# Optimization experiments

Measured on AMD Instinct MI355X. Metric: run time of the kernel, lower is better.

The kernel has to match this reference:

```python
import jax, jax.numpy as jnp
import numpy as np

BUFFER_SIZE = 1024
N_BANDS = 2049
N_SPEC = 4
FRAME_SIZE = 2 * (N_BANDS - 1)  # 4096
EPS = 1e-10


def _hann_periodic(n):
    k = np.arange(n, dtype=np.float64)
    return (0.5 * (1.0 - np.cos(2.0 * np.pi * k / n))).astype(np.float32)


def _build_windows():
    # Mirrors _build_windows with nonlinearity=0 (single filterbank).
    base = _hann_periodic(FRAME_SIZE) / (FRAME_SIZE / 4.0)
    win_scale = float(base.sum())
    wins = [base.copy()]
    for lvl in range(1, N_SPEC):
        stride = 1 << lvl
        small = base[::stride][: FRAME_SIZE // stride]
        w = np.zeros(FRAME_SIZE, dtype=np.float32)
        w[-(FRAME_SIZE // stride):] = small
        w *= win_scale / w.sum()
        wins.append(w)
    return [jnp.asarray(w) for w in wins]


WINDOWS = _build_windows()


def _forward(x):
    # x: (B, BUFFER_SIZE). Fresh (reset) state: time buffers are zeros,
    # spectrogram/left-boundary buffers are +1e6 (identity for min).
    B = x.shape[0]
    T = 1 << (N_SPEC - 1)  # finest time grid = output columns
    out = jnp.full((B, N_BANDS, T), 1.0e6, dtype=x.dtype)
    pad = jnp.zeros((B, FRAME_SIZE), dtype=x.dtype)
    concat = jnp.concatenate([pad, x], axis=-1)  # (B, FRAME_SIZE + BUFFER_SIZE)
    for lvl in range(N_SPEC):
        chunk = BUFFER_SIZE >> lvl
        nfr = 1 << lvl  # sub-frames at this level
        # Overlap-save sliding windows: frame i starts at offset chunk + i*chunk
        frames = jnp.stack(
            [concat[:, chunk + i * chunk: chunk + i * chunk + FRAME_SIZE] for i in range(nfr)],
            axis=1,
        )  # (B, nfr, FRAME_SIZE)
        spec = jnp.fft.rfft(frames * WINDOWS[lvl][None, None, :], n=FRAME_SIZE, axis=-1)
        power = jnp.transpose(spec.real ** 2 + spec.imag ** 2, (0, 2, 1))  # (B, N_BANDS, nfr)
        # Upsample coarse-time levels to the finest grid (tile replication, the
        # streaming moving-max/min buffers realize this in the original) and
        # take the min across scales (buffers initialised to 1e6 = +inf for min).
        out = jnp.minimum(out, jnp.repeat(power, T // nfr, axis=-1))
    return 10.0 * jnp.log10(jnp.maximum(out, EPS))  # power -> dB


def setup_inputs() -> dict:
    key = jax.random.key(0)
    x = jax.random.normal(key, (1024, BUFFER_SIZE), dtype=jnp.float32)
    return {"x": x}


def reference(x):
    return _forward(x)
```

## Files before the change

### kernel.cpp

```cpp
#include <hip/hip_runtime.h>
#include <hip/hip_fp16.h>
#include <math.h>

#define NBANDS 2049
#define NF 4096
#define NC 2048
#define BUF 1024
#define THREADS 512
#define R2C 0.70710678118654752f

__device__ __forceinline__ int SW(int i) { return i ^ (i >> 2) ^ (i >> 6); }

__device__ __forceinline__ int posrev10(int j) {
  return ((j & 3) << 9) | (((j >> 2) & 3) << 7) | (((j >> 4) & 3) << 5) |
         (((j >> 6) & 3) << 3) | (((j >> 8) & 3) << 1);
}

struct Smem {
  alignas(16) float xs[BUF];
  alignas(16) float zre[3][NC];
  alignas(16) float zim[3][NC];
};

struct State {
  float2 W[5];
  float2 Ub;
  float2 U1;
  float so;
  float s1a[5], s1b[5];
  float s2a[5], s2b[5];
  __half2 oh[4][5];
};

__device__ __forceinline__ float2 cmul(float2 a, float2 b) {
  return make_float2(a.x * b.x - a.y * b.y, a.x * b.y + a.y * b.x);
}

template <int L>
__device__ __forceinline__ float cheb(float c) {
  #pragma unroll
  for (int i = 0; i < L; ++i) c = 2.0f * c * c - 1.0f;
  return c;
}

template <int L>
__device__ __forceinline__ void fused_s1(float* __restrict__ re, float* __restrict__ im,
                                         const Smem& sm, const State& st, int off) {
  const int n = threadIdx.x;
  constexpr int M = NF >> L;
  constexpr float ws = (float)(1 << L) * (0.5f / 1024.0f);
  const int lo = 512 - (min(off, M) >> 1);
  float dr = 0.0f, di = 0.0f;
  if (n >= lo) {
    const int idx = 2 * n + off - 1024;
    const float2 xv = *(const float2*)&sm.xs[idx];
    const float cE = cheb<L>(-st.W[0].y);
    const float cO = cheb<L>(st.so);
    dr = ws * (1.0f - cE) * xv.x;
    di = ws * (1.0f - cO) * xv.y;
  }
  const float2 W = st.W[0];
  const float2 W2 = make_float2(W.x * W.x - W.y * W.y, 2.0f * W.x * W.y);
  const float2 W3 = cmul(W, W2);
  const int p0 = SW(n), p1 = SW(n + 512), p2 = SW(n + 1024), p3 = SW(n + 1536);
  re[p0] = dr;                       im[p0] = di;
  re[p1] = -di * W.x - dr * W.y;     im[p1] = -di * W.y + dr * W.x;
  re[p2] = -(dr * W2.x - di * W2.y); im[p2] = -(dr * W2.y + di * W2.x);
  re[p3] =  di * W3.x + dr * W3.y;   im[p3] =  di * W3.y - dr * W3.x;
}

__device__ __forceinline__ void bfly4(float* __restrict__ re, float* __restrict__ im,
                                      int i0, int i1, int i2, int i3,
                                      float2 W, float2 W2, float2 W3) {
  float ar = re[i0], ai = im[i0];
  float br = re[i1], bi = im[i1];
  float cr = re[i2], ci = im[i2];
  float dr = re[i3], di = im[i3];
  float t0r = ar + cr, t0i = ai + ci;
  float t1r = ar - cr, t1i = ai - ci;
  float t2r = br + dr, t2i = bi + di;
  float t3r = br - dr, t3i = bi - di;
  re[i0] = t0r + t2r; im[i0] = t0i + t2i;
  float y1r = t1r + t3i, y1i = t1i - t3r;
  re[i1] = y1r * W.x - y1i * W.y;  im[i1] = y1r * W.y + y1i * W.x;
  float y2r = t0r - t2r, y2i = t0i - t2i;
  re[i2] = y2r * W2.x - y2i * W2.y; im[i2] = y2r * W2.y + y2i * W2.x;
  float y3r = t1r - t3i, y3i = t1i + t3r;
  re[i3] = y3r * W3.x - y3i * W3.y; im[i3] = y3r * W3.y + y3i * W3.x;
}

template <int LM, int NFR>
__device__ __forceinline__ void radix4p(Smem& sm, float2 W) {
  const int j = threadIdx.x;
  const int m = 1 << LM;
  const int base = ((j >> LM) << (LM + 2)) | (j & (m - 1));
  const int i0 = SW(base), i1 = SW(base + m), i2 = SW(base + 2 * m), i3 = SW(base + 3 * m);
  float2 W2 = make_float2(W.x * W.x - W.y * W.y, 2.0f * W.x * W.y);
  float2 W3 = cmul(W, W2);
  #pragma unroll
  for (int f = 0; f < NFR; ++f)
    bfly4(sm.zre[f], sm.zim[f], i0, i1, i2, i3, W, W2, W3);
}

__device__ __forceinline__ void pair_powers(const float* __restrict__ re,
                                            const float* __restrict__ im,
                                            int kp, float2 U, float& pp, float& pm) {
  const int k1 = kp & (NC - 1);
  const int k2 = (NC - kp) & (NC - 1);
  const int q1 = SW(posrev10(k1 & 1023));
  const int q2 = SW(posrev10(k2 & 1023));
  const float s1 = (k1 & 1024) ? -1.0f : 1.0f;
  const float s2 = (k2 & 1024) ? -1.0f : 1.0f;
  const float2 vr1 = *(const float2*)&re[q1 & ~1];
  const float2 vi1 = *(const float2*)&im[q1 & ~1];
  const float2 vr2 = *(const float2*)&re[q2 & ~1];
  const float2 vi2 = *(const float2*)&im[q2 & ~1];
  const bool o1 = (q1 & 1), o2 = (q2 & 1);
  const float zkr = o1 ? (vr1.y + s1 * vr1.x) : (vr1.x + s1 * vr1.y);
  const float zki = o1 ? (vi1.y + s1 * vi1.x) : (vi1.x + s1 * vi1.y);
  const float zmr = o2 ? (vr2.y + s2 * vr2.x) : (vr2.x + s2 * vr2.y);
  const float zmi = o2 ? (vi2.y + s2 * vi2.x) : (vi2.x + s2 * vi2.y);
  const float Ex = 0.5f * (zkr + zmr), Ey = 0.5f * (zki - zmi);
  const float Ox = 0.5f * (zki + zmi), Oy = -0.5f * (zkr - zmr);
  const float Vx = U.x * Ox - U.y * Oy, Vy = U.x * Oy + U.y * Ox;
  const float ax = Ex + Vx, ay = Ey + Vy;
  const float bx = Ex - Vx, by = Ey - Vy;
  pp = ax * ax + ay * ay;
  pm = bx * bx + by * by;
}

template <int ACT, int COL, int SLOT>
__device__ __forceinline__ void act(State& st, float p) {
  if constexpr (ACT == 0)      st.s1a[SLOT] = fminf(p, 1.0e6f);
  else if constexpr (ACT == 1) st.s1b[SLOT] = fminf(p, 1.0e6f);
  else if constexpr (ACT == 2) { st.s1a[SLOT] = fminf(st.s1a[SLOT], p); st.s1b[SLOT] = fminf(st.s1b[SLOT], p); }
  else if constexpr (ACT == 3) st.s2a[SLOT] = fminf(st.s1a[SLOT], p);
  else if constexpr (ACT == 4) st.s2b[SLOT] = fminf(st.s1a[SLOT], p);
  else if constexpr (ACT == 5) st.s2a[SLOT] = fminf(st.s1b[SLOT], p);
  else if constexpr (ACT == 6) st.s2b[SLOT] = fminf(st.s1b[SLOT], p);
  else {
    const float base = (ACT == 7) ? st.s2a[SLOT] : st.s2b[SLOT];
    const float db = 10.0f * log10f(fmaxf(fminf(base, p), 1.0e-10f));
    if constexpr (COL & 1) st.oh[COL >> 1][SLOT].y = __float2half_rn(db);
    else                   st.oh[COL >> 1][SLOT].x = __float2half_rn(db);
  }
}

template <int ACT, int COL>
__device__ __forceinline__ void unpack_frame(const float* __restrict__ re,
                                             const float* __restrict__ im,
                                             State& st) {
  const int t = threadIdx.x;
  float pp, pm;
  pair_powers(re, im, t, st.Ub, pp, pm);
  act<ACT, COL, 0>(st, pp);
  act<ACT, COL, 1>(st, pm);
  pair_powers(re, im, 512 + t, st.U1, pp, pm);
  act<ACT, COL, 2>(st, pp);
  act<ACT, COL, 3>(st, pm);
  if (t == 0) {
    const float zr = re[0] - re[1];
    const float zi = im[0] - im[1];
    act<ACT, COL, 4>(st, zr * zr + zi * zi);
  }
}

template <int LA, int AA, int CA, int LB, int AB, int CB, int LC, int AC, int CC, int NFR>
__device__ __forceinline__ void pass(Smem& sm, State& st, int offA, int offB, int offC) {
  __syncthreads();
  fused_s1<LA>(sm.zre[0], sm.zim[0], sm, st, offA);
  if constexpr (NFR >= 2) fused_s1<LB>(sm.zre[1], sm.zim[1], sm, st, offB);
  if constexpr (NFR >= 3) fused_s1<LC>(sm.zre[2], sm.zim[2], sm, st, offC);
  __syncthreads(); radix4p<7, NFR>(sm, st.W[1]);
  __syncthreads(); radix4p<5, NFR>(sm, st.W[2]);
  __syncthreads(); radix4p<3, NFR>(sm, st.W[3]);
  __syncthreads(); radix4p<1, NFR>(sm, st.W[4]);
  __syncthreads();
  unpack_frame<AA, CA>(sm.zre[0], sm.zim[0], st);
  if constexpr (NFR >= 2) unpack_frame<AB, CB>(sm.zre[1], sm.zim[1], st);
  if constexpr (NFR >= 3) unpack_frame<AC, CC>(sm.zre[2], sm.zim[2], st);
}

__device__ __forceinline__ void store_all(const State& st, float* __restrict__ outb) {
  const int t = threadIdx.x;
  #pragma unroll
  for (int sl = 0; sl < 5; ++sl) {
    if (sl < 4 || t == 0) {
      const int band = (sl == 0) ? t : (sl == 1) ? 2048 - t
                     : (sl == 2) ? 512 + t : (sl == 3) ? 1536 - t : 1024;
      float* bp = outb + (size_t)band * 8;
      *(float4*)(bp)     = make_float4(__half2float(st.oh[0][sl].x), __half2float(st.oh[0][sl].y),
                                       __half2float(st.oh[1][sl].x), __half2float(st.oh[1][sl].y));
      *(float4*)(bp + 4) = make_float4(__half2float(st.oh[2][sl].x), __half2float(st.oh[2][sl].y),
                                       __half2float(st.oh[3][sl].x), __half2float(st.oh[3][sl].y));
    }
  }
}

__global__ __launch_bounds__(THREADS, 2) void spec_kernel(const float* __restrict__ x,
                                                          float* __restrict__ out) {
  __shared__ Smem sm;
  State st;
  const int tid = threadIdx.x;
  const int b = blockIdx.x;
  const float* xb = x + (size_t)b * BUF;
  #pragma unroll
  for (int i = tid; i < BUF; i += THREADS) sm.xs[i] = xb[i];
  {
    float sn, cs;
    sincospif((float)tid * (1.0f / 1024.0f), &sn, &cs);         st.W[0] = make_float2(cs, -sn);
    sincospif((float)(tid & 127) * (1.0f / 256.0f), &sn, &cs);  st.W[1] = make_float2(cs, -sn);
    sincospif((float)(tid & 31) * (1.0f / 64.0f), &sn, &cs);    st.W[2] = make_float2(cs, -sn);
    sincospif((float)(tid & 7) * (1.0f / 16.0f), &sn, &cs);     st.W[3] = make_float2(cs, -sn);
    st.W[4] = (tid & 1) ? make_float2(R2C, -R2C) : make_float2(1.0f, 0.0f);
    sincospif((float)tid * (1.0f / 2048.0f), &sn, &cs);         st.Ub = make_float2(cs, -sn);
    st.U1 = cmul(st.Ub, make_float2(R2C, -R2C));
    sincospif((float)(2 * tid + 1) * (1.0f / 2048.0f), &sn, &cs); st.so = sn;
  }
  float* outb = out + (size_t)b * (NBANDS * 8);

  pass<1, 0, 0,  1, 1, 0,  0, 2, 0, 3>(sm, st, 512, 1024, 1024);
  pass<2, 3, 0,  2, 4, 0,  3, 7, 0, 3>(sm, st, 256, 512, 128);
  pass<3, 7, 1,  3, 8, 2,  3, 8, 3, 3>(sm, st, 256, 384, 512);
  pass<2, 5, 0,  2, 6, 0,  3, 7, 4, 3>(sm, st, 768, 1024, 640);
  pass<3, 7, 5,  3, 8, 6,  3, 8, 7, 3>(sm, st, 768, 896, 1024);
  store_all(st, outb);
}

extern "C" void kernel_launch(void* const* d_in, const int* in_sizes, int n_in,
                              void* d_out, int out_size, void* d_ws, size_t ws_size,
                              hipStream_t stream) {
  const float* x = (const float*)d_in[0];
  float* out = (float*)d_out;
  const int B = in_sizes[0] / BUF;
  hipLaunchKernelGGL(spec_kernel, dim3(B), dim3(THREADS), 0, stream, x, out);
}
```

Before: 109.2 us.

## Process two batch rows per block to amortize FFT barriers and twiddle setup

Each block now handles two input rows: it stages both into shared memory and runs six interleaved FFT frames per pass instead of three. Per-thread twiddle setup and the __syncthreads barriers per radix stage are shared across both rows, and the grid is halved. In exchange, shared memory roughly doubles (about 104 KB per block), register state doubles, and the launch bound drops the minimum of two blocks per CU, so occupancy falls. The launch also assumes an even batch size.

```diff
diff --git a/kernel.cpp b/kernel.cpp
--- a/kernel.cpp
+++ b/kernel.cpp
@@ -17,9 +17,9 @@
 }
 
 struct Smem {
-  alignas(16) float xs[BUF];
-  alignas(16) float zre[3][NC];
-  alignas(16) float zim[3][NC];
+  alignas(16) float xs[2][BUF];
+  alignas(16) float zre[6][NC];
+  alignas(16) float zim[6][NC];
 };
 
 struct State {
@@ -27,9 +27,9 @@
   float2 Ub;
   float2 U1;
   float so;
-  float s1a[5], s1b[5];
-  float s2a[5], s2b[5];
-  __half2 oh[4][5];
+  float s1a[2][5], s1b[2][5];
+  float s2a[2][5], s2b[2][5];
+  __half2 oh[2][4][5];
 };
 
 __device__ __forceinline__ float2 cmul(float2 a, float2 b) {
@@ -45,7 +45,7 @@
 
 template <int L>
 __device__ __forceinline__ void fused_s1(float* __restrict__ re, float* __restrict__ im,
-                                         const Smem& sm, const State& st, int off) {
+                                         const float* __restrict__ xs, const State& st, int off) {
   const int n = threadIdx.x;
   constexpr int M = NF >> L;
   constexpr float ws = (float)(1 << L) * (0.5f / 1024.0f);
@@ -53,7 +53,7 @@
   float dr = 0.0f, di = 0.0f;
   if (n >= lo) {
     const int idx = 2 * n + off - 1024;
-    const float2 xv = *(const float2*)&sm.xs[idx];
+    const float2 xv = *(const float2*)&xs[idx];
     const float cE = cheb<L>(-st.W[0].y);
     const float cO = cheb<L>(st.so);
     dr = ws * (1.0f - cE) * xv.x;
@@ -89,7 +89,7 @@
   re[i3] = y3r * W3.x - y3i * W3.y; im[i3] = y3r * W3.y + y3i * W3.x;
 }
 
-template <int LM, int NFR>
+template <int LM>
 __device__ __forceinline__ void radix4p(Smem& sm, float2 W) {
   const int j = threadIdx.x;
   const int m = 1 << LM;
@@ -98,7 +98,7 @@
   float2 W2 = make_float2(W.x * W.x - W.y * W.y, 2.0f * W.x * W.y);
   float2 W3 = cmul(W, W2);
   #pragma unroll
-  for (int f = 0; f < NFR; ++f)
+  for (int f = 0; f < 6; ++f)
     bfly4(sm.zre[f], sm.zim[f], i0, i1, i2, i3, W, W2, W3);
 }
 
@@ -129,58 +129,65 @@
   pm = bx * bx + by * by;
 }
 
-template <int ACT, int COL, int SLOT>
+template <int ACT, int COL, int SLOT, int ROW>
 __device__ __forceinline__ void act(State& st, float p) {
-  if constexpr (ACT == 0)      st.s1a[SLOT] = fminf(p, 1.0e6f);
-  else if constexpr (ACT == 1) st.s1b[SLOT] = fminf(p, 1.0e6f);
-  else if constexpr (ACT == 2) { st.s1a[SLOT] = fminf(st.s1a[SLOT], p); st.s1b[SLOT] = fminf(st.s1b[SLOT], p); }
-  else if constexpr (ACT == 3) st.s2a[SLOT] = fminf(st.s1a[SLOT], p);
-  else if constexpr (ACT == 4) st.s2b[SLOT] = fminf(st.s1a[SLOT], p);
-  else if constexpr (ACT == 5) st.s2a[SLOT] = fminf(st.s1b[SLOT], p);
-  else if constexpr (ACT == 6) st.s2b[SLOT] = fminf(st.s1b[SLOT], p);
+  if constexpr (ACT == 0)      st.s1a[ROW][SLOT] = fminf(p, 1.0e6f);
+  else if constexpr (ACT == 1) st.s1b[ROW][SLOT] = fminf(p, 1.0e6f);
+  else if constexpr (ACT == 2) { st.s1a[ROW][SLOT] = fminf(st.s1a[ROW][SLOT], p); st.s1b[ROW][SLOT] = fminf(st.s1b[ROW][SLOT], p); }
+  else if constexpr (ACT == 3) st.s2a[ROW][SLOT] = fminf(st.s1a[ROW][SLOT], p);
+  else if constexpr (ACT == 4) st.s2b[ROW][SLOT] = fminf(st.s1a[ROW][SLOT], p);
+  else if constexpr (ACT == 5) st.s2a[ROW][SLOT] = fminf(st.s1b[ROW][SLOT], p);
+  else if constexpr (ACT == 6) st.s2b[ROW][SLOT] = fminf(st.s1b[ROW][SLOT], p);
   else {
-    const float base = (ACT == 7) ? st.s2a[SLOT] : st.s2b[SLOT];
+    const float base = (ACT == 7) ? st.s2a[ROW][SLOT] : st.s2b[ROW][SLOT];
     const float db = 10.0f * log10f(fmaxf(fminf(base, p), 1.0e-10f));
-    if constexpr (COL & 1) st.oh[COL >> 1][SLOT].y = __float2half_rn(db);
-    else                   st.oh[COL >> 1][SLOT].x = __float2half_rn(db);
-  }
-}
-
-template <int ACT, int COL>
+    if constexpr (COL & 1) st.oh[ROW][COL >> 1][SLOT].y = __float2half_rn(db);
+    else                   st.oh[ROW][COL >> 1][SLOT].x = __float2half_rn(db);
+  }
+}
+
+template <int ACT, int COL, int ROW>
 __device__ __forceinline__ void unpack_frame(const float* __restrict__ re,
                                              const float* __restrict__ im,
                                              State& st) {
   const int t = threadIdx.x;
   float pp, pm;
   pair_powers(re, im, t, st.Ub, pp, pm);
-  act<ACT, COL, 0>(st, pp);
-  act<ACT, COL, 1>(st, pm);
+  act<ACT, COL, 0, ROW>(st, pp);
+  act<ACT, COL, 1, ROW>(st, pm);
   pair_powers(re, im, 512 + t, st.U1, pp, pm);
-  act<ACT, COL, 2>(st, pp);
-  act<ACT, COL, 3>(st, pm);
+  act<ACT, COL, 2, ROW>(st, pp);
+  act<ACT, COL, 3, ROW>(st, pm);
   if (t == 0) {
     const float zr = re[0] - re[1];
     const float zi = im[0] - im[1];
-    act<ACT, COL, 4>(st, zr * zr + zi * zi);
-  }
-}
-
-template <int LA, int AA, int CA, int LB, int AB, int CB, int LC, int AC, int CC, int NFR>
+    act<ACT, COL, 4, ROW>(st, zr * zr + zi * zi);
+  }
+}
+
+template <int LA, int AA, int CA, int LB, int AB, int CB, int LC, int AC, int CC>
 __device__ __forceinline__ void pass(Smem& sm, State& st, int offA, int offB, int offC) {
   __syncthreads();
-  fused_s1<LA>(sm.zre[0], sm.zim[0], sm, st, offA);
-  if constexpr (NFR >= 2) fused_s1<LB>(sm.zre[1], sm.zim[1], sm, st, offB);
-  if constexpr (NFR >= 3) fused_s1<LC>(sm.zre[2], sm.zim[2], sm, st, offC);
-  __syncthreads(); radix4p<7, NFR>(sm, st.W[1]);
-  __syncthreads(); radix4p<5, NFR>(sm, st.W[2]);
-  __syncthreads(); radix4p<3, NFR>(sm, st.W[3]);
-  __syncthreads(); radix4p<1, NFR>(sm, st.W[4]);
+  fused_s1<LA>(sm.zre[0], sm.zim[0], sm.xs[0], st, offA);
+  fused_s1<LB>(sm.zre[1], sm.zim[1], sm.xs[0], st, offB);
+  fused_s1<LC>(sm.zre[2], sm.zim[2], sm.xs[0], st, offC);
+  fused_s1<LA>(sm.zre[3], sm.zim[3], sm.xs[1], st, offA);
+  fused_s1<LB>(sm.zre[4], sm.zim[4], sm.xs[1], st, offB);
+  fused_s1<LC>(sm.zre[5], sm.zim[5], sm.xs[1], st, offC);
+  __syncthreads(); radix4p<7>(sm, st.W[1]);
+  __syncthreads(); radix4p<5>(sm, st.W[2]);
+  __syncthreads(); radix4p<3>(sm, st.W[3]);
+  __syncthreads(); radix4p<1>(sm, st.W[4]);
   __syncthreads();
-  unpack_frame<AA, CA>(sm.zre[0], sm.zim[0], st);
-  if constexpr (NFR >= 2) unpack_frame<AB, CB>(sm.zre[1], sm.zim[1], st);
-  if constexpr (NFR >= 3) unpack_frame<AC, CC>(sm.zre[2], sm.zim[2], st);
-}
-
+  unpack_frame<AA, CA, 0>(sm.zre[0], sm.zim[0], st);
+  unpack_frame<AB, CB, 0>(sm.zre[1], sm.zim[1], st);
+  unpack_frame<AC, CC, 0>(sm.zre[2], sm.zim[2], st);
+  unpack_frame<AA, CA, 1>(sm.zre[3], sm.zim[3], st);
+  unpack_frame<AB, CB, 1>(sm.zre[4], sm.zim[4], st);
+  unpack_frame<AC, CC, 1>(sm.zre[5], sm.zim[5], st);
+}
+
+template <int ROW>
 __device__ __forceinline__ void store_all(const State& st, float* __restrict__ outb) {
   const int t = threadIdx.x;
   #pragma unroll
@@ -189,23 +196,23 @@
       const int band = (sl == 0) ? t : (sl == 1) ? 2048 - t
                      : (sl == 2) ? 512 + t : (sl == 3) ? 1536 - t : 1024;
       float* bp = outb + (size_t)band * 8;
-      *(float4*)(bp)     = make_float4(__half2float(st.oh[0][sl].x), __half2float(st.oh[0][sl].y),
-                                       __half2float(st.oh[1][sl].x), __half2float(st.oh[1][sl].y));
-      *(float4*)(bp + 4) = make_float4(__half2float(st.oh[2][sl].x), __half2float(st.oh[2][sl].y),
-                                       __half2float(st.oh[3][sl].x), __half2float(st.oh[3][sl].y));
+      *(float4*)(bp)     = make_float4(__half2float(st.oh[ROW][0][sl].x), __half2float(st.oh[ROW][0][sl].y),
+                                       __half2float(st.oh[ROW][1][sl].x), __half2float(st.oh[ROW][1][sl].y));
+      *(float4*)(bp + 4) = make_float4(__half2float(st.oh[ROW][2][sl].x), __half2float(st.oh[ROW][2][sl].y),
+                                       __half2float(st.oh[ROW][3][sl].x), __half2float(st.oh[ROW][3][sl].y));
     }
   }
 }
 
-__global__ __launch_bounds__(THREADS, 2) void spec_kernel(const float* __restrict__ x,
-                                                          float* __restrict__ out) {
+__global__ __launch_bounds__(THREADS) void spec_kernel(const float* __restrict__ x,
+                                                       float* __restrict__ out) {
   __shared__ Smem sm;
   State st;
   const int tid = threadIdx.x;
   const int b = blockIdx.x;
-  const float* xb = x + (size_t)b * BUF;
-  #pragma unroll
-  for (int i = tid; i < BUF; i += THREADS) sm.xs[i] = xb[i];
+  const float* xb = x + (size_t)(2 * b) * BUF;
+  #pragma unroll
+  for (int i = tid; i < 2 * BUF; i += THREADS) sm.xs[i >> 10][i & (BUF - 1)] = xb[i];
   {
     float sn, cs;
     sincospif((float)tid * (1.0f / 1024.0f), &sn, &cs);         st.W[0] = make_float2(cs, -sn);
@@ -217,14 +224,16 @@
     st.U1 = cmul(st.Ub, make_float2(R2C, -R2C));
     sincospif((float)(2 * tid + 1) * (1.0f / 2048.0f), &sn, &cs); st.so = sn;
   }
-  float* outb = out + (size_t)b * (NBANDS * 8);
-
-  pass<1, 0, 0,  1, 1, 0,  0, 2, 0, 3>(sm, st, 512, 1024, 1024);
-  pass<2, 3, 0,  2, 4, 0,  3, 7, 0, 3>(sm, st, 256, 512, 128);
-  pass<3, 7, 1,  3, 8, 2,  3, 8, 3, 3>(sm, st, 256, 384, 512);
-  pass<2, 5, 0,  2, 6, 0,  3, 7, 4, 3>(sm, st, 768, 1024, 640);
-  pass<3, 7, 5,  3, 8, 6,  3, 8, 7, 3>(sm, st, 768, 896, 1024);
-  store_all(st, outb);
+  float* outb0 = out + (size_t)(2 * b) * (NBANDS * 8);
+  float* outb1 = outb0 + (size_t)(NBANDS * 8);
+
+  pass<1, 0, 0,  1, 1, 0,  0, 2, 0>(sm, st, 512, 1024, 1024);
+  pass<2, 3, 0,  2, 4, 0,  3, 7, 0>(sm, st, 256, 512, 128);
+  pass<3, 7, 1,  3, 8, 2,  3, 8, 3>(sm, st, 256, 384, 512);
+  pass<2, 5, 0,  2, 6, 0,  3, 7, 4>(sm, st, 768, 1024, 640);
+  pass<3, 7, 5,  3, 8, 6,  3, 8, 7>(sm, st, 768, 896, 1024);
+  store_all<0>(st, outb0);
+  store_all<1>(st, outb1);
 }
 
 extern "C" void kernel_launch(void* const* d_in, const int* in_sizes, int n_in,
@@ -233,5 +242,5 @@
   const float* x = (const float*)d_in[0];
   float* out = (float*)d_out;
   const int B = in_sizes[0] / BUF;
-  hipLaunchKernelGGL(spec_kernel, dim3(B), dim3(THREADS), 0, stream, x, out);
-}
+  hipLaunchKernelGGL(spec_kernel, dim3(B / 2), dim3(THREADS), 0, stream, x, out);
+}
```

Result: slower. 187.9 us (+72.1%).
